# Kernel optimization log

Measured on AMD Instinct MI355X. Metric: run time of the kernel, lower is better.

Reference implementation:

```python
import jax, jax.numpy as jnp
import numpy as np

B, T, D, H, L = 128, 512, 512, 512, 256


def setup_inputs() -> dict:
    key = jax.random.key(0)
    ks = jax.random.split(key, 7)
    lim = 1.0 / np.sqrt(H)
    u = lambda k, shape, lo: jax.random.uniform(k, shape, jnp.float32, -lo, lo)
    x = jax.random.normal(ks[0], (B, T, D), dtype=jnp.float32)
    Wih = u(ks[1], (3 * H, D), lim)
    Whh = u(ks[2], (3 * H, H), lim)
    b = u(ks[3], (3 * H,), lim)
    bn = u(ks[4], (H,), lim)
    lim_l = 1.0 / np.sqrt(H)
    Wlin = u(ks[5], (2 * L, H), lim_l)
    blin = u(ks[6], (2 * L,), lim_l)
    return {"x": x, "Wih": Wih, "Whh": Whh, "b": b, "bn": bn, "Wlin": Wlin, "blin": blin}


def reference(x, Wih, Whh, b, bn, Wlin, blin):
    # x: (B, T, D). Batched GRU recurrence over time via lax.scan.
    def step(h, xt):
        ig = xt @ Wih.T + b           # (B, 3H)
        hg = h @ Whh.T                # (B, 3H)
        ir, iz, inn = jnp.split(ig, 3, axis=-1)
        hr, hz, hn = jnp.split(hg, 3, axis=-1)
        r = jax.nn.sigmoid(ir + hr)
        z = jax.nn.sigmoid(iz + hz)
        n = jnp.tanh(inn + r * (hn + bn))
        h_new = (1.0 - z) * n + z * h
        return h_new, None

    xs = jnp.swapaxes(x, 0, 1)        # (T, B, D)
    h0 = jnp.zeros((x.shape[0], Whh.shape[1]), dtype=x.dtype)
    h_final, _ = jax.lax.scan(step, h0, xs)
    out = h_final @ Wlin.T + blin     # (B, 2L)
    mu, logvar = jnp.split(out, 2, axis=-1)
    return (mu, logvar)
```

## Files before the change

kernel.cpp:

```cpp
#include <hip/hip_runtime.h>
#include <stdint.h>


typedef short short8 __attribute__((ext_vector_type(8)));
typedef float f32x4 __attribute__((ext_vector_type(4)));
typedef int int4v __attribute__((ext_vector_type(4)));

#define NB 128
#define NT 512
#define ND 512
#define NH 512
#define NG 1536
#define HSLOT (NB * NH)

__device__ __forceinline__ unsigned short f2bf(float f) {
  union { float f; unsigned u; } v; v.f = f;
  unsigned r = v.u + 0x7fffu + ((v.u >> 16) & 1u);
  return (unsigned short)(r >> 16);
}
__device__ __forceinline__ float bf2f(unsigned short u) {
  union { unsigned u; float f; } v; v.u = ((unsigned)u) << 16; return v.f;
}
__device__ __forceinline__ float sigmoid_f(float x) {
  float e = __builtin_amdgcn_exp2f(-1.4426950408889634f * x);
  return __builtin_amdgcn_rcpf(1.0f + e);
}
__device__ __forceinline__ float tanh_f(float x) {
  float e = __builtin_amdgcn_exp2f(2.8853900817779268f * x);
  return 1.0f - 2.0f * __builtin_amdgcn_rcpf(1.0f + e);
}
__device__ __forceinline__ short8 pack8(float4 a, float4 b) {
  short8 s;
  s[0] = (short)f2bf(a.x); s[1] = (short)f2bf(a.y);
  s[2] = (short)f2bf(a.z); s[3] = (short)f2bf(a.w);
  s[4] = (short)f2bf(b.x); s[5] = (short)f2bf(b.y);
  s[6] = (short)f2bf(b.z); s[7] = (short)f2bf(b.w);
  return s;
}

__device__ __forceinline__ void load16x2_s(const unsigned short* p0,
                                           const unsigned short* p1,
                                           int4v* v0, int4v* v1) {
  asm volatile(
      "global_load_dwordx4 %0, %2, off sc0 sc1\n\t"
      "global_load_dwordx4 %1, %3, off sc0 sc1\n\t"
      "s_waitcnt vmcnt(0)"
      : "=&v"(*v0), "=&v"(*v1) : "v"(p0), "v"(p1) : "memory");
}

__device__ __forceinline__ void store4_s(unsigned short* p, unsigned v0,
                                         unsigned v1, unsigned v2, unsigned v3) {
  asm volatile(
      "global_store_short %0, %1, off sc0 sc1\n\t"
      "global_store_short %0, %2, off offset:1024 sc0 sc1\n\t"
      "global_store_short %0, %3, off offset:2048 sc0 sc1\n\t"
      "global_store_short %0, %4, off offset:3072 sc0 sc1\n\t"
      "s_waitcnt vmcnt(0)"
      :: "v"(p), "v"(v0), "v"(v1), "v"(v2), "v"(v3) : "memory");
}

__device__ __forceinline__ unsigned poll_s(const unsigned* p) {
  unsigned f;
  asm volatile("global_load_dword %0, %1, off sc0 sc1\n\t"
               "s_waitcnt vmcnt(0)" : "=v"(f) : "v"(p) : "memory");
  return f;
}

__device__ __forceinline__ void fstore_s(unsigned* p, unsigned v) {
  asm volatile("global_store_dword %0, %1, off sc0 sc1"
               :: "v"(p), "v"(v) : "memory");
}

__global__ __launch_bounds__(256) void ig_gemm(
    const float* __restrict__ x, const float* __restrict__ Wih,
    const float* __restrict__ bias, unsigned short* __restrict__ IG) {
  __shared__ unsigned short As[128 * 40];
  __shared__ unsigned short Bs[128 * 40];
  const int tid = threadIdx.x;
  const int bn = blockIdx.x, bm = blockIdx.y;
  const int lane = tid & 63, w = tid >> 6;
  const int wm = w >> 1, wn = w & 1;
  const int l15 = lane & 15, q = lane >> 4;

  f32x4 acc[4][4] = {};

  for (int kt = 0; kt < 16; ++kt) {
    __syncthreads();
#pragma unroll
    for (int j = 0; j < 4; ++j) {
      int fi = tid + 256 * j;
      int row = fi >> 3, kq = fi & 7;
      float4 v = *(const float4*)(x + (size_t)(bm * 128 + row) * ND + kt * 32 + kq * 4);
      ushort4 s = {f2bf(v.x), f2bf(v.y), f2bf(v.z), f2bf(v.w)};
      *(ushort4*)&As[row * 40 + kq * 4] = s;
    }
#pragma unroll
    for (int j = 0; j < 4; ++j) {
      int fi = tid + 256 * j;
      int row = fi >> 3, kq = fi & 7;
      float4 v = *(const float4*)(Wih + (size_t)(bn * 128 + row) * ND + kt * 32 + kq * 4);
      ushort4 s = {f2bf(v.x), f2bf(v.y), f2bf(v.z), f2bf(v.w)};
      *(ushort4*)&Bs[row * 40 + kq * 4] = s;
    }
    __syncthreads();

    short8 af[4], bf[4];
#pragma unroll
    for (int tm = 0; tm < 4; ++tm)
      af[tm] = *(const short8*)&As[(wm * 64 + tm * 16 + l15) * 40 + q * 8];
#pragma unroll
    for (int tn = 0; tn < 4; ++tn)
      bf[tn] = *(const short8*)&Bs[(wn * 64 + tn * 16 + l15) * 40 + q * 8];
#pragma unroll
    for (int tm = 0; tm < 4; ++tm)
#pragma unroll
      for (int tn = 0; tn < 4; ++tn)
        acc[tm][tn] = __builtin_amdgcn_mfma_f32_16x16x32_bf16(af[tm], bf[tn], acc[tm][tn], 0, 0, 0);
  }

#pragma unroll
  for (int tm = 0; tm < 4; ++tm) {
#pragma unroll
    for (int tn = 0; tn < 4; ++tn) {
      int col = bn * 128 + wn * 64 + tn * 16 + l15;
      float bb = bias[col];
#pragma unroll
      for (int i = 0; i < 4; ++i) {
        int row = bm * 128 + wm * 64 + tm * 16 + q * 4 + i;
        IG[(size_t)row * NG + col] = f2bf(acc[tm][tn][i] + bb);
      }
    }
  }
}

template <bool USE_IG>
__global__ __launch_bounds__(512, 2) void gru_rec(
    const float* __restrict__ x, const float* __restrict__ Wih,
    const float* __restrict__ Whh, const float* __restrict__ bias,
    const float* __restrict__ bn, const unsigned short* __restrict__ IG,
    unsigned short* __restrict__ hbuf, unsigned* __restrict__ flags,
    float* __restrict__ hfin) {
  __shared__ unsigned short hs[16 * 512];

  const int tid = threadIdx.x;
  const int lane = tid & 63;
  const int w = tid >> 6;
  const int l15 = lane & 15, q = lane >> 4;
  const int bid = blockIdx.x;
  const int g = bid & 7, cblk = bid >> 3;
  const int col = cblk * 128 + w * 16 + l15;
  const int erow = g * 16 + q * 4;
  const int mrow = g * 16 + l15;

  unsigned* const myflag = flags + g * 4 + cblk;
  const unsigned* const pollbase = flags + g * 4;

  short8 bfr[3][16];
#pragma unroll
  for (int gt = 0; gt < 3; ++gt) {
    const float* src = Whh + (size_t)(gt * NH + col) * NH + q * 8;
#pragma unroll
    for (int kk = 0; kk < 16; ++kk) {
      float4 v0 = *(const float4*)(src + kk * 32);
      float4 v1 = *(const float4*)(src + kk * 32 + 4);
      bfr[gt][kk] = pack8(v0, v1);
    }
  }

  float bi_r = 0.f, bi_z = 0.f, bi_n = 0.f;
  if (!USE_IG) {
    bi_r = bias[col];
    bi_z = bias[NH + col];
    bi_n = bias[2 * NH + col];
  }
  const float bnv = bn[col];

  float hreg[4] = {0.f, 0.f, 0.f, 0.f};

  const int s0 = tid * 2;
  const int frow = s0 >> 6;
  const int fsi = s0 & 63;
  const int fr7 = frow & 7;

  for (int t = 0; t < NT; ++t) {
    const unsigned short* hcur = hbuf + (size_t)(t & 1) * HSLOT;
    unsigned short* hnxt = hbuf + (size_t)((t & 1) ^ 1) * HSLOT;

    float igr[4], igz[4], ign[4];
    if (USE_IG) {
#pragma unroll
      for (int i = 0; i < 4; ++i) {
        const size_t base = ((size_t)(erow + i) * NT + t) * NG + col;
        igr[i] = bf2f(IG[base]);
        igz[i] = bf2f(IG[base + NH]);
        ign[i] = bf2f(IG[base + 2 * NH]);
      }
    }

    if (t > 0) {
      if (tid < 4) {
        const unsigned* fp = pollbase + tid;
        unsigned f = poll_s(fp);
        while ((int)f < t) f = poll_s(fp);
      }
      __syncthreads();
    }

    {
      const unsigned short* hrow = hcur + (size_t)(g * 16 + frow) * NH;
      int4v v0, v1;
      load16x2_s(hrow + ((fsi ^ fr7) << 3), hrow + (((fsi + 1) ^ fr7) << 3),
                 &v0, &v1);
      *(int4v*)&hs[frow * 512 + (fsi << 3)] = v0;
      *(int4v*)&hs[frow * 512 + ((fsi + 1) << 3)] = v1;
    }
    __syncthreads();

    f32x4 ar = {0.f, 0.f, 0.f, 0.f};
    f32x4 az = {0.f, 0.f, 0.f, 0.f};
    f32x4 an = {0.f, 0.f, 0.f, 0.f};
    f32x4 ai = {0.f, 0.f, 0.f, 0.f};
    const int abase = l15 * 512;
    const int ar7 = (l15 & 7) << 3;
#pragma unroll
    for (int kk = 0; kk < 16; ++kk) {
      short8 afk = *(const short8*)&hs[abase + ((kk * 32 + q * 8) ^ ar7)];
      ar = __builtin_amdgcn_mfma_f32_16x16x32_bf16(afk, bfr[0][kk], ar, 0, 0, 0);
      az = __builtin_amdgcn_mfma_f32_16x16x32_bf16(afk, bfr[1][kk], az, 0, 0, 0);
      an = __builtin_amdgcn_mfma_f32_16x16x32_bf16(afk, bfr[2][kk], an, 0, 0, 0);
      if (!USE_IG) {
        const float* xp = x + ((size_t)mrow * NT + t) * ND + kk * 32 + q * 8;
        short8 xa = pack8(*(const float4*)xp, *(const float4*)(xp + 4));
#pragma unroll
        for (int gt = 0; gt < 3; ++gt) {
          const float* wp = Wih + (size_t)(gt * NH + col) * ND + kk * 32 + q * 8;
          short8 wf = pack8(*(const float4*)wp, *(const float4*)(wp + 4));
          if (gt == 0) ar = __builtin_amdgcn_mfma_f32_16x16x32_bf16(xa, wf, ar, 0, 0, 0);
          if (gt == 1) az = __builtin_amdgcn_mfma_f32_16x16x32_bf16(xa, wf, az, 0, 0, 0);
          if (gt == 2) ai = __builtin_amdgcn_mfma_f32_16x16x32_bf16(xa, wf, ai, 0, 0, 0);
        }
      }
    }

    unsigned sv[4];
#pragma unroll
    for (int i = 0; i < 4; ++i) {
      float xr = USE_IG ? (ar[i] + igr[i]) : (ar[i] + bi_r);
      float xz = USE_IG ? (az[i] + igz[i]) : (az[i] + bi_z);
      float xin = USE_IG ? ign[i] : (ai[i] + bi_n);
      float r = sigmoid_f(xr);
      float z = sigmoid_f(xz);
      float n = tanh_f(xin + r * (an[i] + bnv));
      float hn2 = (1.f - z) * n + z * hreg[i];
      hreg[i] = hn2;
      sv[i] = (unsigned)f2bf(hn2);
      if (t == NT - 1) hfin[(size_t)(erow + i) * NH + col] = hn2;
    }
    if (t != NT - 1) {
      store4_s(hnxt + (size_t)erow * NH + col, sv[0], sv[1], sv[2], sv[3]);
      __syncthreads();
      if (tid == 0) fstore_s(myflag, (unsigned)(t + 1));
    }
  }
}

__global__ __launch_bounds__(256) void final_linear(
    const float* __restrict__ hfin, const float* __restrict__ Wlin,
    const float* __restrict__ blin, float* __restrict__ out) {
  __shared__ float sh[16 * 516];
  const int tid = threadIdx.x;
  const int b0 = blockIdx.y * 16, o0 = blockIdx.x * 16;

  for (int j = tid; j < 16 * 128; j += 256) {
    int row = j >> 7, kq = j & 127;
    *(float4*)&sh[row * 516 + kq * 4] =
        *(const float4*)(hfin + (size_t)(b0 + row) * NH + kq * 4);
  }
  __syncthreads();

  const int bi = tid & 15, oi = tid >> 4;
  const int o = o0 + oi;
  const float4* wp = (const float4*)(Wlin + (size_t)o * NH);
  float4 a4 = {0.f, 0.f, 0.f, 0.f};
  for (int k4 = 0; k4 < 128; ++k4) {
    float4 wv = wp[k4];
    float4 hv = *(const float4*)&sh[bi * 516 + k4 * 4];
    a4.x += wv.x * hv.x; a4.y += wv.y * hv.y;
    a4.z += wv.z * hv.z; a4.w += wv.w * hv.w;
  }
  float v = a4.x + a4.y + a4.z + a4.w + blin[o];
  int b = b0 + bi;
  if (o < 256) out[b * 256 + o] = v;
  else out[32768 + b * 256 + (o - 256)] = v;
}

extern "C" void kernel_launch(void* const* d_in, const int* in_sizes, int n_in,
                              void* d_out, int out_size, void* d_ws, size_t ws_size,
                              hipStream_t stream) {
  const float* x    = (const float*)d_in[0];
  const float* Wih  = (const float*)d_in[1];
  const float* Whh  = (const float*)d_in[2];
  const float* bias = (const float*)d_in[3];
  const float* bn   = (const float*)d_in[4];
  const float* Wlin = (const float*)d_in[5];
  const float* blin = (const float*)d_in[6];
  float* out = (float*)d_out;

  char* ws = (char*)d_ws;
  unsigned short* hbuf = (unsigned short*)ws;
  unsigned* flags      = (unsigned*)(ws + 262144);
  float* hfin          = (float*)(ws + 263168);
  unsigned short* IG   = (unsigned short*)(ws + 525312);
  const size_t need_min = 525312;
  const size_t need_ig  = need_min + (size_t)NB * NT * NG * 2;
  if (ws_size < need_min) return;

  hipMemsetAsync(ws, 0, 131072, stream);
  hipMemsetAsync(ws + 262144, 0, 1024, stream);

  const bool useIG = (ws_size >= need_ig);
  if (useIG) {
    ig_gemm<<<dim3(12, 512), 256, 0, stream>>>(x, Wih, bias, IG);
    gru_rec<true><<<32, 512, 0, stream>>>(x, Wih, Whh, bias, bn, IG, hbuf, flags, hfin);
  } else {
    gru_rec<false><<<32, 512, 0, stream>>>(x, Wih, Whh, bias, bn, nullptr, hbuf, flags, hfin);
  }
  final_linear<<<dim3(32, 8), 256, 0, stream>>>(hfin, Wlin, blin, out);
}
```

Before: 2.330 ms.

## Stage h outputs in LDS for coalesced stores and reuse own slice locally

```diff
diff --git a/kernel.cpp b/kernel.cpp
--- a/kernel.cpp
+++ b/kernel.cpp
@@ -48,15 +48,11 @@
       : "=&v"(*v0), "=&v"(*v1) : "v"(p0), "v"(p1) : "memory");
 }
 
-__device__ __forceinline__ void store4_s(unsigned short* p, unsigned v0,
-                                         unsigned v1, unsigned v2, unsigned v3) {
+__device__ __forceinline__ void store8_s(unsigned short* p, unsigned long long v) {
   asm volatile(
-      "global_store_short %0, %1, off sc0 sc1\n\t"
-      "global_store_short %0, %2, off offset:1024 sc0 sc1\n\t"
-      "global_store_short %0, %3, off offset:2048 sc0 sc1\n\t"
-      "global_store_short %0, %4, off offset:3072 sc0 sc1\n\t"
+      "global_store_dwordx2 %0, %1, off sc0 sc1\n\t"
       "s_waitcnt vmcnt(0)"
-      :: "v"(p), "v"(v0), "v"(v1), "v"(v2), "v"(v3) : "memory");
+      :: "v"(p), "v"(v) : "memory");
 }
 
 __device__ __forceinline__ unsigned poll_s(const unsigned* p) {
@@ -141,6 +137,7 @@
     unsigned short* __restrict__ hbuf, unsigned* __restrict__ flags,
     float* __restrict__ hfin) {
   __shared__ unsigned short hs[16 * 512];
+  __shared__ unsigned short ts[16 * 128];
 
   const int tid = threadIdx.x;
   const int lane = tid & 63;
@@ -177,10 +174,13 @@
 
   float hreg[4] = {0.f, 0.f, 0.f, 0.f};
 
-  const int s0 = tid * 2;
-  const int frow = s0 >> 6;
-  const int fsi = s0 & 63;
+  const int frow = tid >> 5;
+  const int fsi = (tid & 31) * 2;
   const int fr7 = frow & 7;
+  const bool own_slot = ((fsi >> 4) == cblk);
+
+  const int srow = tid >> 5;
+  const int scol = (tid & 31) * 4;
 
   for (int t = 0; t < NT; ++t) {
     const unsigned short* hcur = hbuf + (size_t)(t & 1) * HSLOT;
@@ -198,7 +198,7 @@
     }
 
     if (t > 0) {
-      if (tid < 4) {
+      if (tid < 4 && tid != cblk) {
         const unsigned* fp = pollbase + tid;
         unsigned f = poll_s(fp);
         while ((int)f < t) f = poll_s(fp);
@@ -206,7 +206,14 @@
       __syncthreads();
     }
 
-    {
+    if (t > 0 && own_slot) {
+      const int ls0 = (fsi ^ fr7) & 15;
+      const int ls1 = ((fsi + 1) ^ fr7) & 15;
+      *(int4v*)&hs[frow * 512 + (fsi << 3)] =
+          *(const int4v*)&ts[frow * 128 + ls0 * 8];
+      *(int4v*)&hs[frow * 512 + ((fsi + 1) << 3)] =
+          *(const int4v*)&ts[frow * 128 + ls1 * 8];
+    } else {
       const unsigned short* hrow = hcur + (size_t)(g * 16 + frow) * NH;
       int4v v0, v1;
       load16x2_s(hrow + ((fsi ^ fr7) << 3), hrow + (((fsi + 1) ^ fr7) << 3),
@@ -242,7 +249,7 @@
       }
     }
 
-    unsigned sv[4];
+    unsigned short sv[4];
 #pragma unroll
     for (int i = 0; i < 4; ++i) {
       float xr = USE_IG ? (ar[i] + igr[i]) : (ar[i] + bi_r);
@@ -253,11 +260,17 @@
       float n = tanh_f(xin + r * (an[i] + bnv));
       float hn2 = (1.f - z) * n + z * hreg[i];
       hreg[i] = hn2;
-      sv[i] = (unsigned)f2bf(hn2);
+      sv[i] = f2bf(hn2);
       if (t == NT - 1) hfin[(size_t)(erow + i) * NH + col] = hn2;
     }
+
     if (t != NT - 1) {
-      store4_s(hnxt + (size_t)erow * NH + col, sv[0], sv[1], sv[2], sv[3]);
+#pragma unroll
+      for (int i = 0; i < 4; ++i)
+        ts[(q * 4 + i) * 128 + w * 16 + l15] = sv[i];
+      __syncthreads();
+      unsigned long long v8 = *(const unsigned long long*)&ts[srow * 128 + scol];
+      store8_s(hnxt + (size_t)(g * 16 + srow) * NH + cblk * 128 + scol, v8);
       __syncthreads();
       if (tid == 0) fstore_s(myflag, (unsigned)(t + 1));
     }
```

Result: no change. 2.363 ms (+1.4%).
